# Kernel tuning notes

Measured on AMD Instinct MI355X. Metric: run time of the kernel, lower is better.

The kernel has to match this reference:

```python
import jax, jax.numpy as jnp
import numpy as np

WINDOW = 128  # window_size from init_kwargs
D = 1024      # input_dim
S = 8192      # seq_len


def setup_inputs() -> dict:
    key = jax.random.key(0)
    k1, k2, k3, k4, k5 = jax.random.split(key, 5)
    bound = 1.0 / np.sqrt(D)
    x = jax.random.normal(k1, (1, S, D), dtype=jnp.float32)
    Wq = jax.random.uniform(k2, (D, D), minval=-bound, maxval=bound, dtype=jnp.float32)
    bq = jax.random.uniform(k3, (D,), minval=-bound, maxval=bound, dtype=jnp.float32)
    Wk = jax.random.uniform(k4, (D, D), minval=-bound, maxval=bound, dtype=jnp.float32)
    bk = jax.random.uniform(k5, (D,), minval=-bound, maxval=bound, dtype=jnp.float32)
    return {"x": x, "Wq": Wq, "bq": bq, "Wk": Wk, "bk": bk}


def reference(x, Wq, bq, Wk, bk):
    # x: [1, S, D]  (original code only works with batch==1)
    xs = x[0]                          # [S, D]
    q = xs @ Wq.T + bq                 # [S, D]
    k = xs @ Wk.T + bk                 # [S, D]
    scores = q @ k.T                   # [S, S] dense, matches original buffer
    t = jnp.arange(S)[:, None]
    s = jnp.arange(S)[None, :]
    # original writes scores only for s in [t-WINDOW, t+WINDOW); elsewhere stays 0
    inwin = (s >= t - WINDOW) & (s < t + WINDOW)
    scores = jnp.where(inwin, scores, 0.0)
    attn = jax.nn.softmax(scores, axis=1)  # softmax INCLUDES the zero entries, as in original
    out = attn @ xs                    # [S, D]
    return out
```

## Files before the change

kernel.cpp:

```cpp
#include <hip/hip_runtime.h>

#define S 8192
#define D 1024
#define WINDOW 128
#define TQ 16
#define UMAX 288
#define BK 32
#define PAD 68
#define BAND 320

typedef __attribute__((ext_vector_type(8))) short short8;
typedef __attribute__((ext_vector_type(4))) float floatx4;
typedef __attribute__((ext_vector_type(4))) unsigned short ushort4v;
typedef unsigned short u16t;

__device__ __forceinline__ float wave_sum(float v) {
  #pragma unroll
  for (int off = 32; off > 0; off >>= 1) v += __shfl_xor(v, off, 64);
  return v;
}
__device__ __forceinline__ float wave_max(float v) {
  #pragma unroll
  for (int off = 32; off > 0; off >>= 1) v = fmaxf(v, __shfl_xor(v, off, 64));
  return v;
}
__device__ __forceinline__ unsigned int f2bf_rn(float f) {
  unsigned int u = __float_as_uint(f);
  return (u + 0x7fffu + ((u >> 16) & 1u)) >> 16;
}

#define GLDS(gp, lp) __builtin_amdgcn_global_load_lds( \
    (const __attribute__((address_space(1))) void*)(gp), \
    (__attribute__((address_space(3))) void*)(lp), 16, 0, 0)


__global__ __launch_bounds__(256) void wuv_kernel(
    const float* __restrict__ Wq, const float* __restrict__ Wk,
    const float* __restrict__ bq, const float* __restrict__ bk,
    float* __restrict__ u, float* __restrict__ v, float* __restrict__ cbuf,
    u16t* __restrict__ wqth, u16t* __restrict__ wqtl,
    u16t* __restrict__ wkth, u16t* __restrict__ wktl)
{
  __shared__ float tile[64][65];
  const int t = threadIdx.x;
  if (blockIdx.z == 2) {
    if (blockIdx.x >= 4 || blockIdx.y >= 8) return;
    const int i = blockIdx.x * 256 + t;
    const int n0 = blockIdx.y * 128;
    float us = 0.f, vs = 0.f;
    for (int n = n0; n < n0 + 128; ++n) {
      us += Wq[(size_t)n * D + i] * bk[n];
      vs += Wk[(size_t)n * D + i] * bq[n];
    }
    atomicAdd(&u[i], us);
    atomicAdd(&v[i], vs);
    if (blockIdx.x == 0 && blockIdx.y == 0) {
      float cs = 0.f;
      for (int n = t; n < D; n += 256) cs += bq[n] * bk[n];
      atomicAdd(cbuf, cs);
    }
    return;
  }
  const float* W = blockIdx.z ? Wk : Wq;
  u16t* oh = blockIdx.z ? wkth : wqth;
  u16t* ol = blockIdx.z ? wktl : wqtl;
  const int n0 = blockIdx.x * 64;
  const int i0 = blockIdx.y * 64;
  #pragma unroll
  for (int p = 0; p < 4; ++p) {
    int r = (t >> 4) + p * 16;
    int c = (t & 15) * 4;
    float4 vv = *(const float4*)(W + (size_t)(n0 + r) * D + i0 + c);
    tile[r][c+0] = vv.x; tile[r][c+1] = vv.y; tile[r][c+2] = vv.z; tile[r][c+3] = vv.w;
  }
  __syncthreads();
  #pragma unroll
  for (int p = 0; p < 4; ++p) {
    int ii = (t >> 4) + p * 16;
    int nn = (t & 15) * 4;
    ushort4v h, l;
    #pragma unroll
    for (int e = 0; e < 4; ++e) {
      float f = tile[nn + e][ii];
      unsigned int hb = f2bf_rn(f);
      float hf = __uint_as_float(hb << 16);
      h[e] = (u16t)hb;
      l[e] = (u16t)f2bf_rn(f - hf);
    }
    size_t idx = (size_t)(i0 + ii) * D + n0 + nn;
    *(ushort4v*)(oh + idx) = h;
    *(ushort4v*)(ol + idx) = l;
  }
}

__global__ __launch_bounds__(256) void prep_kernel(
    const float* __restrict__ x, const float* __restrict__ u,
    const float* __restrict__ v, u16t* __restrict__ xhi, u16t* __restrict__ xlo,
    u16t* __restrict__ xT, float* __restrict__ xsum,
    float* __restrict__ a, float* __restrict__ b)
{
  __shared__ float tile[64][65];
  const int s0 = blockIdx.x * 64;
  const int d0 = blockIdx.y * 64;
  const int t = threadIdx.x;
  #pragma unroll
  for (int p = 0; p < 4; ++p) {
    int r = (t >> 4) + p * 16;
    int c = (t & 15) * 4;
    float4 vv = *(const float4*)(x + (size_t)(s0 + r) * D + d0 + c);
    float f[4] = {vv.x, vv.y, vv.z, vv.w};
    tile[r][c+0] = vv.x; tile[r][c+1] = vv.y; tile[r][c+2] = vv.z; tile[r][c+3] = vv.w;
    ushort4v h, l;
    #pragma unroll
    for (int e = 0; e < 4; ++e) {
      unsigned int hb = f2bf_rn(f[e]);
      float hf = __uint_as_float(hb << 16);
      h[e] = (u16t)hb;
      l[e] = (u16t)f2bf_rn(f[e] - hf);
    }
    size_t idx = (size_t)(s0 + r) * D + d0 + c;
    *(ushort4v*)(xhi + idx) = h;
    *(ushort4v*)(xlo + idx) = l;
  }
  __syncthreads();
  #pragma unroll
  for (int p = 0; p < 4; ++p) {
    int dd = (t >> 4) + p * 16;
    int ss = (t & 15) * 4;
    ushort4v o;
    #pragma unroll
    for (int e = 0; e < 4; ++e) o[e] = (u16t)f2bf_rn(tile[ss + e][dd]);
    *(ushort4v*)(xT + (size_t)(d0 + dd) * S + s0 + ss) = o;
  }
  if (t < 64) {
    float s = 0.f;
    #pragma unroll 8
    for (int r = 0; r < 64; ++r) s += tile[r][t];
    atomicAdd(&xsum[d0 + t], s);
  } else if (t < 128) {
    int r = t - 64;
    float s = 0.f;
    for (int c = 0; c < 64; ++c) s += tile[r][c] * u[d0 + c];
    atomicAdd(&a[s0 + r], s);
  } else if (t < 192) {
    int r = t - 128;
    float s = 0.f;
    for (int c = 0; c < 64; ++c) s += tile[r][c] * v[d0 + c];
    atomicAdd(&b[s0 + r], s);
  }
}

__global__ __launch_bounds__(256) void m_kernel(
    const u16t* __restrict__ wqth, const u16t* __restrict__ wqtl,
    const u16t* __restrict__ wkth, const u16t* __restrict__ wktl,
    u16t* __restrict__ mh, u16t* __restrict__ ml)
{
  __shared__ __align__(16) u16t Mbuf[4][64 * BK];

  const int tid  = threadIdx.x;
  const int lane = tid & 63;
  const int wv   = tid >> 6;
  const int i0   = blockIdx.x * 64;
  const int j0   = blockIdx.y * 64;

  floatx4 acc[2][2] = {};
  const int m0w = (wv & 1) * 32;
  const int n0w = (wv >> 1) * 32;
  const int srow = lane >> 2;
  const int scolw = ((lane & 3) ^ ((lane >> 3) & 3)) * 8;
  const int rs    = (((lane >> 4) ^ ((lane >> 1) & 3)) * 8);

  for (int k0 = 0; k0 < D; k0 += BK) {
    __syncthreads();
    {
      const u16t* src = (wv == 0) ? wqth : (wv == 1) ? wqtl : (wv == 2) ? wkth : wktl;
      const int base  = (wv < 2) ? i0 : j0;
      #pragma unroll
      for (int sg = 0; sg < 4; ++sg) {
        int row = base + sg * 16 + srow;
        size_t g = (size_t)row * D + k0 + scolw;
        GLDS(src + g, &Mbuf[wv][sg * 512]);
      }
    }
    __syncthreads();
    short8 ah[2], al[2], bh[2], bl[2];
    #pragma unroll
    for (int t = 0; t < 2; ++t) {
      int ar = (m0w + t * 16 + (lane & 15)) * BK + rs;
      int br = (n0w + t * 16 + (lane & 15)) * BK + rs;
      ah[t] = *(const short8*)&Mbuf[0][ar];
      al[t] = *(const short8*)&Mbuf[1][ar];
      bh[t] = *(const short8*)&Mbuf[2][br];
      bl[t] = *(const short8*)&Mbuf[3][br];
    }
    #pragma unroll
    for (int mt = 0; mt < 2; ++mt)
      #pragma unroll
      for (int nt = 0; nt < 2; ++nt) {
        acc[mt][nt] = __builtin_amdgcn_mfma_f32_16x16x32_bf16(ah[mt], bh[nt], acc[mt][nt], 0, 0, 0);
        acc[mt][nt] = __builtin_amdgcn_mfma_f32_16x16x32_bf16(ah[mt], bl[nt], acc[mt][nt], 0, 0, 0);
        acc[mt][nt] = __builtin_amdgcn_mfma_f32_16x16x32_bf16(al[mt], bh[nt], acc[mt][nt], 0, 0, 0);
      }
  }
  #pragma unroll
  for (int mt = 0; mt < 2; ++mt)
    #pragma unroll
    for (int nt = 0; nt < 2; ++nt) {
      int j = j0 + n0w + nt * 16 + (lane & 15);
      int i = i0 + m0w + mt * 16 + (lane >> 4) * 4;
      #pragma unroll
      for (int r = 0; r < 4; ++r) {
        float f = acc[mt][nt][r];
        unsigned int hb = f2bf_rn(f);
        float hf = __uint_as_float(hb << 16);
        size_t idx = (size_t)(i + r) * D + j;
        mh[idx] = (u16t)hb;
        ml[idx] = (u16t)f2bf_rn(f - hf);
      }
    }
}

__global__ __launch_bounds__(256) void y_kernel(
    const u16t* __restrict__ xhi, const u16t* __restrict__ xlo,
    const u16t* __restrict__ mhp, const u16t* __restrict__ mlp,
    u16t* __restrict__ yh, u16t* __restrict__ yl)
{
  __shared__ __align__(16) u16t Ah[2 * 128 * BK];
  __shared__ __align__(16) u16t Al[2 * 128 * BK];
  __shared__ __align__(16) u16t Bh[2 * 128 * BK];
  __shared__ __align__(16) u16t Bl[2 * 128 * BK];

  const int tid  = threadIdx.x;
  const int lane = tid & 63;
  const int wv   = tid >> 6;
  const int s0   = blockIdx.x * 128;
  const int i0   = blockIdx.y * 128;

  floatx4 acc[4][4] = {};
  const int m0w  = (wv & 1) * 64;
  const int n0w  = (wv >> 1) * 64;
  const int srow = lane >> 2;
  const int scolw = ((lane & 3) ^ ((lane >> 3) & 3)) * 8;
  const int rs    = (((lane >> 4) ^ ((lane >> 1) & 3)) * 8);

  for (int k0 = 0; k0 < D; k0 += 64) {
    __syncthreads();
    #pragma unroll
    for (int h = 0; h < 2; ++h) {
      #pragma unroll
      for (int sg = 0; sg < 2; ++sg) {
        int seg  = wv * 2 + sg;
        int arow = s0 + seg * 16 + srow;
        int brow = i0 + seg * 16 + srow;
        size_t ga = (size_t)arow * D + k0 + h * 32 + scolw;
        size_t gb = (size_t)brow * D + k0 + h * 32 + scolw;
        int lb = h * 4096 + seg * 512;
        GLDS(xhi + ga, &Ah[lb]);
        GLDS(xlo + ga, &Al[lb]);
        GLDS(mhp + gb, &Bh[lb]);
        GLDS(mlp + gb, &Bl[lb]);
      }
    }
    __syncthreads();
    #pragma unroll
    for (int h = 0; h < 2; ++h) {
      short8 ah[4], al[4], bh[4], bl[4];
      #pragma unroll
      for (int t = 0; t < 4; ++t) {
        int ar = h * 4096 + (m0w + t * 16 + (lane & 15)) * BK + rs;
        int br = h * 4096 + (n0w + t * 16 + (lane & 15)) * BK + rs;
        ah[t] = *(const short8*)&Ah[ar];
        al[t] = *(const short8*)&Al[ar];
        bh[t] = *(const short8*)&Bh[br];
        bl[t] = *(const short8*)&Bl[br];
      }
      #pragma unroll
      for (int mt = 0; mt < 4; ++mt)
        #pragma unroll
        for (int nt = 0; nt < 4; ++nt) {
          acc[mt][nt] = __builtin_amdgcn_mfma_f32_16x16x32_bf16(ah[mt], bh[nt], acc[mt][nt], 0, 0, 0);
          acc[mt][nt] = __builtin_amdgcn_mfma_f32_16x16x32_bf16(ah[mt], bl[nt], acc[mt][nt], 0, 0, 0);
          acc[mt][nt] = __builtin_amdgcn_mfma_f32_16x16x32_bf16(al[mt], bh[nt], acc[mt][nt], 0, 0, 0);
        }
    }
  }
  #pragma unroll
  for (int mt = 0; mt < 4; ++mt)
    #pragma unroll
    for (int nt = 0; nt < 4; ++nt) {
      int i = i0 + n0w + nt * 16 + (lane & 15);
      int s = s0 + m0w + mt * 16 + (lane >> 4) * 4;
      #pragma unroll
      for (int r = 0; r < 4; ++r) {
        float f = acc[mt][nt][r];
        unsigned int hb = f2bf_rn(f);
        float hf = __uint_as_float(hb << 16);
        size_t idx = (size_t)(s + r) * D + i;
        yh[idx] = (u16t)hb;
        yl[idx] = (u16t)f2bf_rn(f - hf);
      }
    }
}

__global__ __launch_bounds__(256) void scores_kernel(
    const u16t* __restrict__ xhi, const u16t* __restrict__ xlo,
    const u16t* __restrict__ yh, const u16t* __restrict__ yl,
    const float* __restrict__ a, const float* __restrict__ b,
    const float* __restrict__ cbuf, float* __restrict__ band)
{
  __shared__ __align__(16) u16t Ah[2 * 64 * BK];
  __shared__ __align__(16) u16t Al[2 * 64 * BK];
  __shared__ __align__(16) u16t Bh[2 * 64 * BK];
  __shared__ __align__(16) u16t Bl[2 * 64 * BK];

  const int tid  = threadIdx.x;
  const int lane = tid & 63;
  const int wv   = tid >> 6;
  const int t0   = blockIdx.x * 64;
  const int jt   = blockIdx.y;
  const int s_base = t0 - 128 + jt * 64;
  const float cval = cbuf[0];

  floatx4 acc[2][2] = {};
  const int m0w  = (wv & 1) * 32;
  const int n0w  = (wv >> 1) * 32;
  const int srow = lane >> 2;
  const int scolw = ((lane & 3) ^ ((lane >> 3) & 3)) * 8;
  const int rs    = (((lane >> 4) ^ ((lane >> 1) & 3)) * 8);

  for (int k0 = 0; k0 < D; k0 += 64) {
    __syncthreads();
    #pragma unroll
    for (int h = 0; h < 2; ++h) {
      int arow = t0 + wv * 16 + srow;
      int brow = s_base + wv * 16 + srow;
      brow = min(max(brow, 0), S - 1);
      size_t ga = (size_t)arow * D + k0 + h * 32 + scolw;
      size_t gb = (size_t)brow * D + k0 + h * 32 + scolw;
      int lb = h * 2048 + wv * 512;
      GLDS(xhi + ga, &Ah[lb]);
      GLDS(xlo + ga, &Al[lb]);
      GLDS(yh + gb, &Bh[lb]);
      GLDS(yl + gb, &Bl[lb]);
    }
    __syncthreads();
    #pragma unroll
    for (int h = 0; h < 2; ++h) {
      short8 ah[2], al[2], bh[2], bl[2];
      #pragma unroll
      for (int t = 0; t < 2; ++t) {
        int ar = h * 2048 + (m0w + t * 16 + (lane & 15)) * BK + rs;
        int br = h * 2048 + (n0w + t * 16 + (lane & 15)) * BK + rs;
        ah[t] = *(const short8*)&Ah[ar];
        al[t] = *(const short8*)&Al[ar];
        bh[t] = *(const short8*)&Bh[br];
        bl[t] = *(const short8*)&Bl[br];
      }
      #pragma unroll
      for (int mt = 0; mt < 2; ++mt)
        #pragma unroll
        for (int nt = 0; nt < 2; ++nt) {
          acc[mt][nt] = __builtin_amdgcn_mfma_f32_16x16x32_bf16(ah[mt], bh[nt], acc[mt][nt], 0, 0, 0);
          acc[mt][nt] = __builtin_amdgcn_mfma_f32_16x16x32_bf16(ah[mt], bl[nt], acc[mt][nt], 0, 0, 0);
          acc[mt][nt] = __builtin_amdgcn_mfma_f32_16x16x32_bf16(al[mt], bh[nt], acc[mt][nt], 0, 0, 0);
        }
    }
  }
  #pragma unroll
  for (int mt = 0; mt < 2; ++mt)
    #pragma unroll
    for (int nt = 0; nt < 2; ++nt) {
      int n_loc = n0w + nt * 16 + (lane & 15);
      int s = s_base + n_loc;
      float bv = (s >= 0 && s < S) ? b[s] : 0.f;
      #pragma unroll
      for (int r = 0; r < 4; ++r) {
        int m_loc = m0w + mt * 16 + (lane >> 4) * 4 + r;
        int t = t0 + m_loc;
        bool inwin = (s >= t - WINDOW) && (s < t + WINDOW) && (s >= 0) && (s < S);
        float sv = inwin ? (acc[mt][nt][r] + a[t] + bv + cval) : 0.f;
        band[(size_t)t * BAND + jt * 64 + n_loc] = sv;
      }
    }
}

__global__ __launch_bounds__(256) void softmax_kernel(
    const float* __restrict__ band, u16t* __restrict__ Pb, float* __restrict__ e0d)
{
  const int lane = threadIdx.x & 63;
  const int w    = threadIdx.x >> 6;
  const int t    = blockIdx.x * 4 + w;
  const float* row = band + (size_t)t * BAND;
  float v[5];
  float mx = 0.f;
  #pragma unroll
  for (int i = 0; i < 5; ++i) {
    v[i] = row[i * 64 + lane];
    mx = fmaxf(mx, v[i]);
  }
  mx = wave_max(mx);
  float e0 = __expf(-mx);
  float ss = 0.f;
  #pragma unroll
  for (int i = 0; i < 5; ++i) {
    v[i] = __expf(v[i] - mx);
    ss += v[i];
  }
  ss = wave_sum(ss);
  float dinv = 1.f / (ss + (float)(S - BAND) * e0);
  #pragma unroll
  for (int i = 0; i < 5; ++i)
    Pb[(size_t)t * BAND + i * 64 + lane] = (u16t)f2bf_rn((v[i] - e0) * dinv);
  if (lane == 0) e0d[t] = e0 * dinv;
}

__global__ __launch_bounds__(256) void pv_kernel(
    const u16t* __restrict__ Pb, const u16t* __restrict__ xT,
    const float* __restrict__ e0d, const float* __restrict__ xsum,
    float* __restrict__ out)
{
  __shared__ __align__(16) u16t Ab[2 * 64 * BK];
  __shared__ __align__(16) u16t Bb[2 * 128 * BK];

  const int tid  = threadIdx.x;
  const int lane = tid & 63;
  const int wv   = tid >> 6;
  const int t0   = blockIdx.x * 64;
  const int d0   = blockIdx.y * 128;
  const int origin = t0 - 128;

  floatx4 acc[2][4] = {};
  const int m0w  = (wv & 1) * 32;
  const int n0w  = (wv >> 1) * 64;
  const int srow = lane >> 2;
  const int scolw = ((lane & 3) ^ ((lane >> 3) & 3)) * 8;
  const int rs    = (((lane >> 4) ^ ((lane >> 1) & 3)) * 8);

  for (int k0 = 0; k0 < BAND; k0 += 64) {
    __syncthreads();
    #pragma unroll
    for (int h = 0; h < 2; ++h) {
      {
        int arow = t0 + wv * 16 + srow;
        size_t ga = (size_t)arow * BAND + k0 + h * 32 + scolw;
        int lb = h * 2048 + wv * 512;
        GLDS(Pb + ga, &Ab[lb]);
      }
      #pragma unroll
      for (int sg = 0; sg < 2; ++sg) {
        int seg  = wv * 2 + sg;
        int brow = d0 + seg * 16 + srow;
        int s_g  = origin + k0 + h * 32 + scolw;
        s_g = min(max(s_g, 0), S - 8);
        size_t gb = (size_t)brow * S + s_g;
        int lb = h * 4096 + seg * 512;
        GLDS(xT + gb, &Bb[lb]);
      }
    }
    __syncthreads();
    #pragma unroll
    for (int h = 0; h < 2; ++h) {
      short8 af[2], bf[4];
      #pragma unroll
      for (int t = 0; t < 2; ++t) {
        int ar = h * 2048 + (m0w + t * 16 + (lane & 15)) * BK + rs;
        af[t] = *(const short8*)&Ab[ar];
      }
      #pragma unroll
      for (int t = 0; t < 4; ++t) {
        int br = h * 4096 + (n0w + t * 16 + (lane & 15)) * BK + rs;
        bf[t] = *(const short8*)&Bb[br];
      }
      #pragma unroll
      for (int mt = 0; mt < 2; ++mt)
        #pragma unroll
        for (int nt = 0; nt < 4; ++nt)
          acc[mt][nt] = __builtin_amdgcn_mfma_f32_16x16x32_bf16(af[mt], bf[nt], acc[mt][nt], 0, 0, 0);
    }
  }
  #pragma unroll
  for (int mt = 0; mt < 2; ++mt)
    #pragma unroll
    for (int nt = 0; nt < 4; ++nt) {
      int n_g = d0 + n0w + nt * 16 + (lane & 15);
      float xs = xsum[n_g];
      #pragma unroll
      for (int r = 0; r < 4; ++r) {
        int m_g = t0 + m0w + mt * 16 + (lane >> 4) * 4 + r;
        out[(size_t)m_g * D + n_g] = acc[mt][nt][r] + e0d[m_g] * xs;
      }
    }
}

__global__ __launch_bounds__(256) void proj_kernel(
    const float* __restrict__ x, const float* __restrict__ Wq,
    const float* __restrict__ bqv, const float* __restrict__ Wk,
    const float* __restrict__ bkv, float* __restrict__ qout,
    float* __restrict__ kout)
{
  __shared__ __align__(16) float xs[BK][PAD];
  __shared__ __align__(16) float wqs[BK][PAD];
  __shared__ __align__(16) float wks[BK][PAD];
  const int tid = threadIdx.x;
  const int tx = tid & 15, ty = tid >> 4;
  const int t0 = blockIdx.x * 64, i0 = blockIdx.y * 64;
  float accq[4][4] = {}, acck[4][4] = {};
  const int lrow0 = tid >> 3, lc4 = (tid & 7) * 4;
  for (int k0 = 0; k0 < D; k0 += BK) {
    __syncthreads();
    #pragma unroll
    for (int p = 0; p < 2; ++p) {
      int row = lrow0 + p * 32;
      float4 a = *(const float4*)(x  + (size_t)(t0 + row) * D + k0 + lc4);
      float4 b = *(const float4*)(Wq + (size_t)(i0 + row) * D + k0 + lc4);
      float4 c = *(const float4*)(Wk + (size_t)(i0 + row) * D + k0 + lc4);
      xs [lc4+0][row]=a.x; xs [lc4+1][row]=a.y; xs [lc4+2][row]=a.z; xs [lc4+3][row]=a.w;
      wqs[lc4+0][row]=b.x; wqs[lc4+1][row]=b.y; wqs[lc4+2][row]=b.z; wqs[lc4+3][row]=b.w;
      wks[lc4+0][row]=c.x; wks[lc4+1][row]=c.y; wks[lc4+2][row]=c.z; wks[lc4+3][row]=c.w;
    }
    __syncthreads();
    #pragma unroll
    for (int kk = 0; kk < BK; ++kk) {
      float4 av = *(const float4*)&xs [kk][ty*4];
      float4 bv = *(const float4*)&wqs[kk][tx*4];
      float4 cv = *(const float4*)&wks[kk][tx*4];
      float a[4] = {av.x, av.y, av.z, av.w};
      float b[4] = {bv.x, bv.y, bv.z, bv.w};
      float c[4] = {cv.x, cv.y, cv.z, cv.w};
      #pragma unroll
      for (int r = 0; r < 4; ++r)
        #pragma unroll
        for (int cc = 0; cc < 4; ++cc) {
          accq[r][cc] = fmaf(a[r], b[cc], accq[r][cc]);
          acck[r][cc] = fmaf(a[r], c[cc], acck[r][cc]);
        }
    }
  }
  float4 bq4 = *(const float4*)(bqv + i0 + tx*4);
  float4 bk4 = *(const float4*)(bkv + i0 + tx*4);
  #pragma unroll
  for (int r = 0; r < 4; ++r) {
    int trow = t0 + ty*4 + r;
    float4 oq = { accq[r][0]+bq4.x, accq[r][1]+bq4.y, accq[r][2]+bq4.z, accq[r][3]+bq4.w };
    float4 ok = { acck[r][0]+bk4.x, acck[r][1]+bk4.y, acck[r][2]+bk4.z, acck[r][3]+bk4.w };
    *(float4*)(qout + (size_t)trow * D + i0 + tx*4) = oq;
// ... 109 lines not shown
          acc[ti].z = fmaf(wvv[u], xr[u].z, acc[ti].z);
          acc[ti].w = fmaf(wvv[u], xr[u].w, acc[ti].w);
        }
      }
    }
    float4 xsv = *(const float4*)(xsum + c4);
    #pragma unroll
    for (int ti = 0; ti < TQ; ++ti) {
      float e0 = e0s[ti], di = dinv[ti];
      float4 o;
      o.x = (acc[ti].x + e0 * xsv.x) * di;
      o.y = (acc[ti].y + e0 * xsv.y) * di;
      o.z = (acc[ti].z + e0 * xsv.z) * di;
      o.w = (acc[ti].w + e0 * xsv.w) * di;
      *(float4*)(out + (size_t)(t0 + ti) * D + c4) = o;
    }
  }
}

extern "C" void kernel_launch(void* const* d_in, const int* in_sizes, int n_in,
                              void* d_out, int out_size, void* d_ws, size_t ws_size,
                              hipStream_t stream) {
  const float* x  = (const float*)d_in[0];
  const float* Wq = (const float*)d_in[1];
  const float* bq = (const float*)d_in[2];
  const float* Wk = (const float*)d_in[3];
  const float* bk = (const float*)d_in[4];
  float* outp = (float*)d_out;

  const size_t SD = (size_t)S * D;
  const size_t DD = (size_t)D * D;

  float* xsum = (float*)d_ws;
  float* u    = xsum + D;
  float* v    = u + D;
  float* a    = v + D;
  float* b    = a + S;
  float* cbuf = b + S;
  size_t zero_bytes = (size_t)(3 * D + 2 * S + 16) * sizeof(float);

  u16t* xhi  = (u16t*)(cbuf + 16);
  u16t* xlo  = xhi + SD;
  u16t* xT   = xlo + SD;
  u16t* wqth = xT + SD;
  u16t* wqtl = wqth + DD;
  u16t* wkth = wqtl + DD;
  u16t* wktl = wkth + DD;
  u16t* mh   = wktl + DD;
  u16t* ml   = mh + DD;
  u16t* yh   = ml + DD;
  u16t* yl   = yh + SD;
  float* band = (float*)(yl + SD);
  u16t*  Pb   = (u16t*)(band + (size_t)S * BAND);
  float* e0d  = (float*)(Pb + (size_t)S * BAND);
  size_t needed = (size_t)((char*)(e0d + S) - (char*)d_ws);

  if (ws_size >= needed) {
    (void)hipMemsetAsync(d_ws, 0, zero_bytes, stream);
    wuv_kernel<<<dim3(D / 64, D / 64, 3), 256, 0, stream>>>(
        Wq, Wk, bq, bk, u, v, cbuf, wqth, wqtl, wkth, wktl);
    prep_kernel<<<dim3(S / 64, D / 64), 256, 0, stream>>>(x, u, v, xhi, xlo, xT, xsum, a, b);
    m_kernel<<<dim3(D / 64, D / 64), 256, 0, stream>>>(wqth, wqtl, wkth, wktl, mh, ml);
    y_kernel<<<dim3(S / 128, D / 128), 256, 0, stream>>>(xhi, xlo, mh, ml, yh, yl);
    scores_kernel<<<dim3(S / 64, 5), 256, 0, stream>>>(xhi, xlo, yh, yl, a, b, cbuf, band);
    softmax_kernel<<<S / 4, 256, 0, stream>>>(band, Pb, e0d);
    pv_kernel<<<dim3(S / 64, D / 128), 256, 0, stream>>>(Pb, xT, e0d, xsum, outp);
  } else {
    float* xs2  = (float*)d_ws;
    float* q    = xs2 + D;
    float* kbuf = q + SD;
    (void)hipMemsetAsync(xs2, 0, D * sizeof(float), stream);
    colsum_kernel<<<dim3(D / 256, S / 256), 256, 0, stream>>>(x, xs2);
    proj_kernel<<<dim3(S / 64, D / 64), 256, 0, stream>>>(x, Wq, bq, Wk, bk, q, kbuf);
    attn_kernel<<<S / TQ, 256, 0, stream>>>(x, q, kbuf, xs2, outp);
  }
}
```

Measured before the change: 261.0 us.

## Fuse pipeline stages into one persistent cooperative kernel with grid syncs

Replaces the memset and seven separate kernel launches with a single cooperative persistent kernel of 512 blocks that loops over virtual block indices for each stage, separated by grid-wide syncs. Zeroing moves in-kernel and the m/uv stage is scheduled alongside the transpose stage differently. The aim is to remove launch gaps and tail effects between the short stages. In exchange, the 64KB shared buffer and two-blocks-per-CU bound may reduce occupancy for stages that previously used less LDS, and grid syncs add barrier cost; the separate launches remain as a fallback if the cooperative launch fails.

```diff
diff --git a/kernel.cpp b/kernel.cpp
--- a/kernel.cpp
+++ b/kernel.cpp
@@ -1,4 +1,7 @@
 #include <hip/hip_runtime.h>
+#include <hip/hip_cooperative_groups.h>
+
+namespace cg = cooperative_groups;
 
 #define S 8192
 #define D 1024
@@ -14,6 +17,14 @@
 typedef __attribute__((ext_vector_type(4))) unsigned short ushort4v;
 typedef unsigned short u16t;
 
+struct Params {
+  const float *x, *Wq, *bq, *Wk, *bk;
+  float *out;
+  float *xsum, *u, *v, *a, *b, *cbuf;
+  u16t *xhi, *xlo, *xT, *wqth, *wqtl, *wkth, *wktl, *mh, *ml, *yh, *yl;
+  float *band; u16t *Pb; float *e0d;
+};
+
 __device__ __forceinline__ float wave_sum(float v) {
   #pragma unroll
   for (int off = 32; off > 0; off >>= 1) v += __shfl_xor(v, off, 64);
@@ -34,49 +45,48 @@
     (__attribute__((address_space(3))) void*)(lp), 16, 0, 0)
 
 
-__global__ __launch_bounds__(256) void wuv_kernel(
-    const float* __restrict__ Wq, const float* __restrict__ Wk,
-    const float* __restrict__ bq, const float* __restrict__ bk,
-    float* __restrict__ u, float* __restrict__ v, float* __restrict__ cbuf,
-    u16t* __restrict__ wqth, u16t* __restrict__ wqtl,
-    u16t* __restrict__ wkth, u16t* __restrict__ wktl)
-{
-  __shared__ float tile[64][65];
-  const int t = threadIdx.x;
-  if (blockIdx.z == 2) {
-    if (blockIdx.x >= 4 || blockIdx.y >= 8) return;
-    const int i = blockIdx.x * 256 + t;
-    const int n0 = blockIdx.y * 128;
-    float us = 0.f, vs = 0.f;
-    for (int n = n0; n < n0 + 128; ++n) {
-      us += Wq[(size_t)n * D + i] * bk[n];
-      vs += Wk[(size_t)n * D + i] * bq[n];
-    }
-    atomicAdd(&u[i], us);
-    atomicAdd(&v[i], vs);
-    if (blockIdx.x == 0 && blockIdx.y == 0) {
-      float cs = 0.f;
-      for (int n = t; n < D; n += 256) cs += bq[n] * bk[n];
-      atomicAdd(cbuf, cs);
-    }
-    return;
-  }
-  const float* W = blockIdx.z ? Wk : Wq;
-  u16t* oh = blockIdx.z ? wkth : wqth;
-  u16t* ol = blockIdx.z ? wktl : wqtl;
-  const int n0 = blockIdx.x * 64;
-  const int i0 = blockIdx.y * 64;
-  #pragma unroll
-  for (int p = 0; p < 4; ++p) {
-    int r = (t >> 4) + p * 16;
+
+static __device__ __forceinline__ void zero_body(const Params& p, int zb, int tid) {
+  const int total = 3 * D + 2 * S + 16;
+  for (int i = zb * 256 + tid; i < total; i += 32 * 256) p.xsum[i] = 0.f;
+}
+
+static __device__ __forceinline__ void uv_body(const Params& p, int bx, int by, int tid) {
+  const int i = bx * 256 + tid;
+  const int n0 = by * 128;
+  float us = 0.f, vs = 0.f;
+  for (int n = n0; n < n0 + 128; ++n) {
+    us += p.Wq[(size_t)n * D + i] * p.bk[n];
+    vs += p.Wk[(size_t)n * D + i] * p.bq[n];
+  }
+  atomicAdd(&p.u[i], us);
+  atomicAdd(&p.v[i], vs);
+  if (bx == 0 && by == 0) {
+    float cs = 0.f;
+    for (int n = tid; n < D; n += 256) cs += p.bq[n] * p.bk[n];
+    atomicAdd(p.cbuf, cs);
+  }
+}
+
+static __device__ __forceinline__ void transW_body(
+    const float* __restrict__ W, u16t* __restrict__ oh, u16t* __restrict__ ol,
+    void* sm, int bx, int by, int t)
+{
+  float (*tile)[65] = reinterpret_cast<float (*)[65]>(sm);
+  const int n0 = bx * 64;
+  const int i0 = by * 64;
+  __syncthreads();
+  #pragma unroll
+  for (int pp = 0; pp < 4; ++pp) {
+    int r = (t >> 4) + pp * 16;
     int c = (t & 15) * 4;
     float4 vv = *(const float4*)(W + (size_t)(n0 + r) * D + i0 + c);
     tile[r][c+0] = vv.x; tile[r][c+1] = vv.y; tile[r][c+2] = vv.z; tile[r][c+3] = vv.w;
   }
   __syncthreads();
   #pragma unroll
-  for (int p = 0; p < 4; ++p) {
-    int ii = (t >> 4) + p * 16;
+  for (int pp = 0; pp < 4; ++pp) {
+    int ii = (t >> 4) + pp * 16;
     int nn = (t & 15) * 4;
     ushort4v h, l;
     #pragma unroll
@@ -93,21 +103,18 @@
   }
 }
 
-__global__ __launch_bounds__(256) void prep_kernel(
-    const float* __restrict__ x, const float* __restrict__ u,
-    const float* __restrict__ v, u16t* __restrict__ xhi, u16t* __restrict__ xlo,
-    u16t* __restrict__ xT, float* __restrict__ xsum,
-    float* __restrict__ a, float* __restrict__ b)
-{
-  __shared__ float tile[64][65];
-  const int s0 = blockIdx.x * 64;
-  const int d0 = blockIdx.y * 64;
-  const int t = threadIdx.x;
-  #pragma unroll
-  for (int p = 0; p < 4; ++p) {
-    int r = (t >> 4) + p * 16;
+static __device__ __forceinline__ void prep_body(const Params& p, void* sm,
+                                                 int bx, int by, int t)
+{
+  float (*tile)[65] = reinterpret_cast<float (*)[65]>(sm);
+  const int s0 = bx * 64;
+  const int d0 = by * 64;
+  __syncthreads();
+  #pragma unroll
+  for (int pp = 0; pp < 4; ++pp) {
+    int r = (t >> 4) + pp * 16;
     int c = (t & 15) * 4;
-    float4 vv = *(const float4*)(x + (size_t)(s0 + r) * D + d0 + c);
+    float4 vv = *(const float4*)(p.x + (size_t)(s0 + r) * D + d0 + c);
     float f[4] = {vv.x, vv.y, vv.z, vv.w};
     tile[r][c+0] = vv.x; tile[r][c+1] = vv.y; tile[r][c+2] = vv.z; tile[r][c+3] = vv.w;
     ushort4v h, l;
@@ -119,49 +126,45 @@
       l[e] = (u16t)f2bf_rn(f[e] - hf);
     }
     size_t idx = (size_t)(s0 + r) * D + d0 + c;
-    *(ushort4v*)(xhi + idx) = h;
-    *(ushort4v*)(xlo + idx) = l;
+    *(ushort4v*)(p.xhi + idx) = h;
+    *(ushort4v*)(p.xlo + idx) = l;
   }
   __syncthreads();
   #pragma unroll
-  for (int p = 0; p < 4; ++p) {
-    int dd = (t >> 4) + p * 16;
+  for (int pp = 0; pp < 4; ++pp) {
+    int dd = (t >> 4) + pp * 16;
     int ss = (t & 15) * 4;
     ushort4v o;
     #pragma unroll
     for (int e = 0; e < 4; ++e) o[e] = (u16t)f2bf_rn(tile[ss + e][dd]);
-    *(ushort4v*)(xT + (size_t)(d0 + dd) * S + s0 + ss) = o;
+    *(ushort4v*)(p.xT + (size_t)(d0 + dd) * S + s0 + ss) = o;
   }
   if (t < 64) {
     float s = 0.f;
     #pragma unroll 8
     for (int r = 0; r < 64; ++r) s += tile[r][t];
-    atomicAdd(&xsum[d0 + t], s);
+    atomicAdd(&p.xsum[d0 + t], s);
   } else if (t < 128) {
     int r = t - 64;
     float s = 0.f;
-    for (int c = 0; c < 64; ++c) s += tile[r][c] * u[d0 + c];
-    atomicAdd(&a[s0 + r], s);
+    for (int c = 0; c < 64; ++c) s += tile[r][c] * p.u[d0 + c];
+    atomicAdd(&p.a[s0 + r], s);
   } else if (t < 192) {
     int r = t - 128;
     float s = 0.f;
-    for (int c = 0; c < 64; ++c) s += tile[r][c] * v[d0 + c];
-    atomicAdd(&b[s0 + r], s);
-  }
-}
-
-__global__ __launch_bounds__(256) void m_kernel(
-    const u16t* __restrict__ wqth, const u16t* __restrict__ wqtl,
-    const u16t* __restrict__ wkth, const u16t* __restrict__ wktl,
-    u16t* __restrict__ mh, u16t* __restrict__ ml)
-{
-  __shared__ __align__(16) u16t Mbuf[4][64 * BK];
-
-  const int tid  = threadIdx.x;
+    for (int c = 0; c < 64; ++c) s += tile[r][c] * p.v[d0 + c];
+    atomicAdd(&p.b[s0 + r], s);
+  }
+}
+
+static __device__ __forceinline__ void m_body(const Params& p, void* sm,
+                                              int bx, int by, int tid)
+{
+  u16t (*Mbuf)[64 * BK] = reinterpret_cast<u16t (*)[64 * BK]>(sm);
   const int lane = tid & 63;
   const int wv   = tid >> 6;
-  const int i0   = blockIdx.x * 64;
-  const int j0   = blockIdx.y * 64;
+  const int i0   = bx * 64;
+  const int j0   = by * 64;
 
   floatx4 acc[2][2] = {};
   const int m0w = (wv & 1) * 32;
@@ -173,7 +176,7 @@
   for (int k0 = 0; k0 < D; k0 += BK) {
     __syncthreads();
     {
-      const u16t* src = (wv == 0) ? wqth : (wv == 1) ? wqtl : (wv == 2) ? wkth : wktl;
+      const u16t* src = (wv == 0) ? p.wqth : (wv == 1) ? p.wqtl : (wv == 2) ? p.wkth : p.wktl;
       const int base  = (wv < 2) ? i0 : j0;
       #pragma unroll
       for (int sg = 0; sg < 4; ++sg) {
@@ -214,27 +217,24 @@
         unsigned int hb = f2bf_rn(f);
         float hf = __uint_as_float(hb << 16);
         size_t idx = (size_t)(i + r) * D + j;
-        mh[idx] = (u16t)hb;
-        ml[idx] = (u16t)f2bf_rn(f - hf);
-      }
-    }
-}
-
-__global__ __launch_bounds__(256) void y_kernel(
-    const u16t* __restrict__ xhi, const u16t* __restrict__ xlo,
-    const u16t* __restrict__ mhp, const u16t* __restrict__ mlp,
-    u16t* __restrict__ yh, u16t* __restrict__ yl)
-{
-  __shared__ __align__(16) u16t Ah[2 * 128 * BK];
-  __shared__ __align__(16) u16t Al[2 * 128 * BK];
-  __shared__ __align__(16) u16t Bh[2 * 128 * BK];
-  __shared__ __align__(16) u16t Bl[2 * 128 * BK];
-
-  const int tid  = threadIdx.x;
+        p.mh[idx] = (u16t)hb;
+        p.ml[idx] = (u16t)f2bf_rn(f - hf);
+      }
+    }
+}
+
+static __device__ __forceinline__ void y_body(const Params& p, void* sm,
+                                              int bx, int by, int tid)
+{
+  u16t* Ah = (u16t*)sm;
+  u16t* Al = Ah + 8192;
+  u16t* Bh = Al + 8192;
+  u16t* Bl = Bh + 8192;
+
   const int lane = tid & 63;
   const int wv   = tid >> 6;
-  const int s0   = blockIdx.x * 128;
-  const int i0   = blockIdx.y * 128;
+  const int s0   = bx * 128;
+  const int i0   = by * 128;
 
   floatx4 acc[4][4] = {};
   const int m0w  = (wv & 1) * 64;
@@ -255,10 +255,10 @@
         size_t ga = (size_t)arow * D + k0 + h * 32 + scolw;
         size_t gb = (size_t)brow * D + k0 + h * 32 + scolw;
         int lb = h * 4096 + seg * 512;
-        GLDS(xhi + ga, &Ah[lb]);
-        GLDS(xlo + ga, &Al[lb]);
-        GLDS(mhp + gb, &Bh[lb]);
-        GLDS(mlp + gb, &Bl[lb]);
+        GLDS(p.xhi + ga, &Ah[lb]);
+        GLDS(p.xlo + ga, &Al[lb]);
+        GLDS(p.mh  + gb, &Bh[lb]);
+        GLDS(p.ml  + gb, &Bl[lb]);
       }
     }
     __syncthreads();
@@ -296,30 +296,25 @@
         unsigned int hb = f2bf_rn(f);
         float hf = __uint_as_float(hb << 16);
         size_t idx = (size_t)(s + r) * D + i;
-        yh[idx] = (u16t)hb;
-        yl[idx] = (u16t)f2bf_rn(f - hf);
-      }
-    }
-}
-
-__global__ __launch_bounds__(256) void scores_kernel(
-    const u16t* __restrict__ xhi, const u16t* __restrict__ xlo,
-    const u16t* __restrict__ yh, const u16t* __restrict__ yl,
-    const float* __restrict__ a, const float* __restrict__ b,
-    const float* __restrict__ cbuf, float* __restrict__ band)
-{
-  __shared__ __align__(16) u16t Ah[2 * 64 * BK];
-  __shared__ __align__(16) u16t Al[2 * 64 * BK];
-  __shared__ __align__(16) u16t Bh[2 * 64 * BK];
-  __shared__ __align__(16) u16t Bl[2 * 64 * BK];
-
-  const int tid  = threadIdx.x;
+        p.yh[idx] = (u16t)hb;
+        p.yl[idx] = (u16t)f2bf_rn(f - hf);
+      }
+    }
+}
+
+static __device__ __forceinline__ void scores_body(const Params& p, void* sm,
+                                                   int bx, int jt, int tid)
+{
+  u16t* Ah = (u16t*)sm;
+  u16t* Al = Ah + 4096;
+  u16t* Bh = Al + 4096;
+  u16t* Bl = Bh + 4096;
+
   const int lane = tid & 63;
   const int wv   = tid >> 6;
-  const int t0   = blockIdx.x * 64;
-  const int jt   = blockIdx.y;
+  const int t0   = bx * 64;
   const int s_base = t0 - 128 + jt * 64;
-  const float cval = cbuf[0];
+  const float cval = p.cbuf[0];
 
   floatx4 acc[2][2] = {};
   const int m0w  = (wv & 1) * 32;
@@ -338,10 +333,10 @@
       size_t ga = (size_t)arow * D + k0 + h * 32 + scolw;
       size_t gb = (size_t)brow * D + k0 + h * 32 + scolw;
       int lb = h * 2048 + wv * 512;
-      GLDS(xhi + ga, &Ah[lb]);
-      GLDS(xlo + ga, &Al[lb]);
-      GLDS(yh + gb, &Bh[lb]);
-      GLDS(yl + gb, &Bl[lb]);
+      GLDS(p.xhi + ga, &Ah[lb]);
+      GLDS(p.xlo + ga, &Al[lb]);
+      GLDS(p.yh  + gb, &Bh[lb]);
+      GLDS(p.yl  + gb, &Bl[lb]);
     }
     __syncthreads();
     #pragma unroll
@@ -372,25 +367,24 @@
     for (int nt = 0; nt < 2; ++nt) {
       int n_loc = n0w + nt * 16 + (lane & 15);
       int s = s_base + n_loc;
-      float bv = (s >= 0 && s < S) ? b[s] : 0.f;
+      float bv = (s >= 0 && s < S) ? p.b[s] : 0.f;
       #pragma unroll
       for (int r = 0; r < 4; ++r) {
         int m_loc = m0w + mt * 16 + (lane >> 4) * 4 + r;
         int t = t0 + m_loc;
         bool inwin = (s >= t - WINDOW) && (s < t + WINDOW) && (s >= 0) && (s < S);
-        float sv = inwin ? (acc[mt][nt][r] + a[t] + bv + cval) : 0.f;
-        band[(size_t)t * BAND + jt * 64 + n_loc] = sv;
-      }
-    }
-}
-
-__global__ __launch_bounds__(256) void softmax_kernel(
-    const float* __restrict__ band, u16t* __restrict__ Pb, float* __restrict__ e0d)
-{
-  const int lane = threadIdx.x & 63;
-  const int w    = threadIdx.x >> 6;
-  const int t    = blockIdx.x * 4 + w;
-  const float* row = band + (size_t)t * BAND;
+        float sv = inwin ? (acc[mt][nt][r] + p.a[t] + bv + cval) : 0.f;
+        p.band[(size_t)t * BAND + jt * 64 + n_loc] = sv;
+      }
+    }
+}
+
+static __device__ __forceinline__ void softmax_body(const Params& p, int vb, int tid)
+{
+  const int lane = tid & 63;
+  const int w    = tid >> 6;
+  const int t    = vb * 4 + w;
+  const float* row = p.band + (size_t)t * BAND;
   float v[5];
   float mx = 0.f;
   #pragma unroll
@@ -410,23 +404,20 @@
   float dinv = 1.f / (ss + (float)(S - BAND) * e0);
   #pragma unroll
   for (int i = 0; i < 5; ++i)
-    Pb[(size_t)t * BAND + i * 64 + lane] = (u16t)f2bf_rn((v[i] - e0) * dinv);
-  if (lane == 0) e0d[t] = e0 * dinv;
-}
-
-__global__ __launch_bounds__(256) void pv_kernel(
-    const u16t* __restrict__ Pb, const u16t* __restrict__ xT,
-    const float* __restrict__ e0d, const float* __restrict__ xsum,
-    float* __restrict__ out)
-{
-  __shared__ __align__(16) u16t Ab[2 * 64 * BK];
-  __shared__ __align__(16) u16t Bb[2 * 128 * BK];
-
-  const int tid  = threadIdx.x;
+    p.Pb[(size_t)t * BAND + i * 64 + lane] = (u16t)f2bf_rn((v[i] - e0) * dinv);
+  if (lane == 0) p.e0d[t] = e0 * dinv;
+}
+
+static __device__ __forceinline__ void pv_body(const Params& p, void* sm,
+                                               int bx, int by, int tid)
+{
+  u16t* Ab = (u16t*)sm;
+  u16t* Bb = Ab + 4096;
+
   const int lane = tid & 63;
   const int wv   = tid >> 6;
-  const int t0   = blockIdx.x * 64;
-  const int d0   = blockIdx.y * 128;
+  const int t0   = bx * 64;
+  const int d0   = by * 128;
   const int origin = t0 - 128;
 
   floatx4 acc[2][4] = {};
@@ -444,7 +435,7 @@
         int arow = t0 + wv * 16 + srow;
         size_t ga = (size_t)arow * BAND + k0 + h * 32 + scolw;
         int lb = h * 2048 + wv * 512;
-        GLDS(Pb + ga, &Ab[lb]);
+        GLDS(p.Pb + ga, &Ab[lb]);
       }
       #pragma unroll
       for (int sg = 0; sg < 2; ++sg) {
@@ -454,7 +445,7 @@
         s_g = min(max(s_g, 0), S - 8);
         size_t gb = (size_t)brow * S + s_g;
         int lb = h * 4096 + seg * 512;
-        GLDS(xT + gb, &Bb[lb]);
+        GLDS(p.xT + gb, &Bb[lb]);
       }
     }
     __syncthreads();
@@ -483,13 +474,75 @@
     #pragma unroll
     for (int nt = 0; nt < 4; ++nt) {
       int n_g = d0 + n0w + nt * 16 + (lane & 15);
-      float xs = xsum[n_g];
+      float xs = p.xsum[n_g];
       #pragma unroll
       for (int r = 0; r < 4; ++r) {
         int m_g = t0 + m0w + mt * 16 + (lane >> 4) * 4 + r;
-        out[(size_t)m_g * D + n_g] = acc[mt][nt][r] + e0d[m_g] * xs;
-      }
-    }
+        p.out[(size_t)m_g * D + n_g] = acc[mt][nt][r] + p.e0d[m_g] * xs;
+      }
+    }
+}
+
+__global__ __launch_bounds__(256, 2) void mega_kernel(Params p)
+{
+  __shared__ __align__(16) unsigned char sm[65536];
+  cg::grid_group grid = cg::this_grid();
+  const int tid = threadIdx.x;
+  const int NB  = gridDim.x;
+
+  for (int vb = blockIdx.x; vb < 544; vb += NB) {
+    if (vb < 256)      transW_body(p.Wq, p.wqth, p.wqtl, sm, vb & 15, vb >> 4, tid);
+    else if (vb < 512) transW_body(p.Wk, p.wkth, p.wktl, sm, (vb - 256) & 15, (vb - 256) >> 4, tid);
+    else               zero_body(p, vb - 512, tid);
+  }
+  grid.sync();
+  for (int vb = blockIdx.x; vb < 288; vb += NB) {
+    if (vb < 256) m_body(p, sm, vb & 15, vb >> 4, tid);
+    else          uv_body(p, (vb - 256) & 3, (vb - 256) >> 2, tid);
+  }
+  grid.sync();
+  for (int vb = blockIdx.x; vb < 2048; vb += NB) prep_body(p, sm, vb & 127, vb >> 7, tid);
+  grid.sync();
+  for (int vb = blockIdx.x; vb < 512; vb += NB) y_body(p, sm, vb & 63, vb >> 6, tid);
+  grid.sync();
+  for (int vb = blockIdx.x; vb < 640; vb += NB) scores_body(p, sm, vb & 127, vb >> 7, tid);
+  grid.sync();
+  for (int vb = blockIdx.x; vb < 2048; vb += NB) softmax_body(p, vb, tid);
+  grid.sync();
+  for (int vb = blockIdx.x; vb < 1024; vb += NB) pv_body(p, sm, vb & 127, vb >> 7, tid);
+}
+
+__global__ __launch_bounds__(256) void wuv_g(Params p) {
+  __shared__ __align__(16) unsigned char sm[64 * 65 * 4 + 16];
+  if (blockIdx.z == 2) {
+    if (blockIdx.x < 4 && blockIdx.y < 8) uv_body(p, blockIdx.x, blockIdx.y, threadIdx.x);
+    return;
+  }
+  if (blockIdx.z == 1) transW_body(p.Wk, p.wkth, p.wktl, sm, blockIdx.x, blockIdx.y, threadIdx.x);
+  else                 transW_body(p.Wq, p.wqth, p.wqtl, sm, blockIdx.x, blockIdx.y, threadIdx.x);
+}
+__global__ __launch_bounds__(256) void prep_g(Params p) {
+  __shared__ __align__(16) unsigned char sm[64 * 65 * 4 + 16];
+  prep_body(p, sm, blockIdx.x, blockIdx.y, threadIdx.x);
+}
+__global__ __launch_bounds__(256) void m_g(Params p) {
+  __shared__ __align__(16) unsigned char sm[4 * 64 * BK * 2];
+  m_body(p, sm, blockIdx.x, blockIdx.y, threadIdx.x);
+}
+__global__ __launch_bounds__(256) void y_g(Params p) {
+  __shared__ __align__(16) unsigned char sm[65536];
+  y_body(p, sm, blockIdx.x, blockIdx.y, threadIdx.x);
+}
+__global__ __launch_bounds__(256) void scores_g(Params p) {
+  __shared__ __align__(16) unsigned char sm[32768];
+  scores_body(p, sm, blockIdx.x, blockIdx.y, threadIdx.x);
+}
+__global__ __launch_bounds__(256) void softmax_g(Params p) {
+  softmax_body(p, blockIdx.x, threadIdx.x);
+}
+__global__ __launch_bounds__(256) void pv_g(Params p) {
+  __shared__ __align__(16) unsigned char sm[24576];
+  pv_body(p, sm, blockIdx.x, blockIdx.y, threadIdx.x);
 }
 
 __global__ __launch_bounds__(256) void proj_kernel(
@@ -509,8 +562,8 @@
   for (int k0 = 0; k0 < D; k0 += BK) {
     __syncthreads();
     #pragma unroll
-    for (int p = 0; p < 2; ++p) {
-      int row = lrow0 + p * 32;
+    for (int pp = 0; pp < 2; ++pp) {
+      int row = lrow0 + pp * 32;
       float4 a = *(const float4*)(x  + (size_t)(t0 + row) * D + k0 + lc4);
       float4 b = *(const float4*)(Wq + (size_t)(i0 + row) * D + k0 + lc4);
       float4 c = *(const float4*)(Wk + (size_t)(i0 + row) * D + k0 + lc4);
@@ -710,15 +763,28 @@
   size_t needed = (size_t)((char*)(e0d + S) - (char*)d_ws);
 
   if (ws_size >= needed) {
-    (void)hipMemsetAsync(d_ws, 0, zero_bytes, stream);
-    wuv_kernel<<<dim3(D / 64, D / 64, 3), 256, 0, stream>>>(
-        Wq, Wk, bq, bk, u, v, cbuf, wqth, wqtl, wkth, wktl);
-    prep_kernel<<<dim3(S / 64, D / 64), 256, 0, stream>>>(x, u, v, xhi, xlo, xT, xsum, a, b);
-    m_kernel<<<dim3(D / 64, D / 64), 256, 0, stream>>>(wqth, wqtl, wkth, wktl, mh, ml);
-    y_kernel<<<dim3(S / 128, D / 128), 256, 0, stream>>>(xhi, xlo, mh, ml, yh, yl);
-    scores_kernel<<<dim3(S / 64, 5), 256, 0, stream>>>(xhi, xlo, yh, yl, a, b, cbuf, band);
-    softmax_kernel<<<S / 4, 256, 0, stream>>>(band, Pb, e0d);
-    pv_kernel<<<dim3(S / 64, D / 128), 256, 0, stream>>>(Pb, xT, e0d, xsum, outp);
+    Params P;
+    P.x = x; P.Wq = Wq; P.bq = bq; P.Wk = Wk; P.bk = bk; P.out = outp;
+    P.xsum = xsum; P.u = u; P.v = v; P.a = a; P.b = b; P.cbuf = cbuf;
+    P.xhi = xhi; P.xlo = xlo; P.xT = xT;
+    P.wqth = wqth; P.wqtl = wqtl; P.wkth = wkth; P.wktl = wktl;
+    P.mh = mh; P.ml = ml; P.yh = yh; P.yl = yl;
+    P.band = band; P.Pb = Pb; P.e0d = e0d;
+
+    void* kargs[] = { (void*)&P };
+    hipError_t ce = hipLaunchCooperativeKernel(
+        (const void*)mega_kernel, dim3(512), dim3(256), kargs, 0, stream);
+    if (ce != hipSuccess) {
+      (void)hipGetLastError();
+      (void)hipMemsetAsync(d_ws, 0, zero_bytes, stream);
+      wuv_g<<<dim3(16, 16, 3), 256, 0, stream>>>(P);
+      prep_g<<<dim3(128, 16), 256, 0, stream>>>(P);
+      m_g<<<dim3(16, 16), 256, 0, stream>>>(P);
+      y_g<<<dim3(64, 8), 256, 0, stream>>>(P);
+      scores_g<<<dim3(128, 5), 256, 0, stream>>>(P);
+      softmax_g<<<2048, 256, 0, stream>>>(P);
+      pv_g<<<dim3(128, 8), 256, 0, stream>>>(P);
+    }
   } else {
     float* xs2  = (float*)d_ws;
     float* q    = xs2 + D;
```

Result: slower. 641.0 us (+145.6%).

## Fuse softmax into PV kernel and fold memset into wuv kernel

Applied to the files above, without the earlier changes.

Drops the separate softmax kernel. Each PV block now computes softmax for its 64 rows straight from the fp32 band and writes the bf16 probabilities into LDS, so the Pb and e0d round trip through global memory and one launch go away. The memset is also removed. wuv_kernel zeroes xsum, a and b, writes u and v as two non-atomic partial sums that prep_kernel adds together, and writes the bias constant directly. The cost is that softmax is recomputed in each of the 8 d-column blocks, and the pv_kernel needs about 42KB of LDS, which may lower its occupancy.

```diff
diff --git a/kernel.cpp b/kernel.cpp
--- a/kernel.cpp
+++ b/kernel.cpp
@@ -37,27 +37,38 @@
 __global__ __launch_bounds__(256) void wuv_kernel(
     const float* __restrict__ Wq, const float* __restrict__ Wk,
     const float* __restrict__ bq, const float* __restrict__ bk,
-    float* __restrict__ u, float* __restrict__ v, float* __restrict__ cbuf,
+    float* __restrict__ uu, float* __restrict__ vv, float* __restrict__ cbuf,
     u16t* __restrict__ wqth, u16t* __restrict__ wqtl,
-    u16t* __restrict__ wkth, u16t* __restrict__ wktl)
+    u16t* __restrict__ wkth, u16t* __restrict__ wktl,
+    float* __restrict__ zreg)
 {
   __shared__ float tile[64][65];
+  __shared__ float cr[4];
   const int t = threadIdx.x;
   if (blockIdx.z == 2) {
-    if (blockIdx.x >= 4 || blockIdx.y >= 8) return;
-    const int i = blockIdx.x * 256 + t;
-    const int n0 = blockIdx.y * 128;
-    float us = 0.f, vs = 0.f;
-    for (int n = n0; n < n0 + 128; ++n) {
-      us += Wq[(size_t)n * D + i] * bk[n];
-      vs += Wk[(size_t)n * D + i] * bq[n];
-    }
-    atomicAdd(&u[i], us);
-    atomicAdd(&v[i], vs);
-    if (blockIdx.x == 0 && blockIdx.y == 0) {
-      float cs = 0.f;
-      for (int n = t; n < D; n += 256) cs += bq[n] * bk[n];
-      atomicAdd(cbuf, cs);
+    if (blockIdx.y == 0) {
+      if (blockIdx.x < 8) {
+        const int i  = (blockIdx.x & 3) * 256 + t;
+        const int nh = blockIdx.x >> 2;
+        float us = 0.f, vs = 0.f;
+        for (int n = nh * 512; n < nh * 512 + 512; ++n) {
+          us += Wq[(size_t)n * D + i] * bk[n];
+          vs += Wk[(size_t)n * D + i] * bq[n];
+        }
+        uu[(size_t)nh * D + i] = us;
+        vv[(size_t)nh * D + i] = vs;
+      } else if (blockIdx.x == 8) {
+        float cs = 0.f;
+        for (int n = t; n < D; n += 256) cs += bq[n] * bk[n];
+        cs = wave_sum(cs);
+        if ((t & 63) == 0) cr[t >> 6] = cs;
+        __syncthreads();
+        if (t == 0) cbuf[0] = cr[0] + cr[1] + cr[2] + cr[3];
+      }
+    } else {
+      int fb  = (blockIdx.y - 1) * 16 + blockIdx.x;
+      int idx = fb * 256 + t;
+      if (idx < D + 2 * S) zreg[idx] = 0.f;
     }
     return;
   }
@@ -70,8 +81,8 @@
   for (int p = 0; p < 4; ++p) {
     int r = (t >> 4) + p * 16;
     int c = (t & 15) * 4;
-    float4 vv = *(const float4*)(W + (size_t)(n0 + r) * D + i0 + c);
-    tile[r][c+0] = vv.x; tile[r][c+1] = vv.y; tile[r][c+2] = vv.z; tile[r][c+3] = vv.w;
+    float4 vf = *(const float4*)(W + (size_t)(n0 + r) * D + i0 + c);
+    tile[r][c+0] = vf.x; tile[r][c+1] = vf.y; tile[r][c+2] = vf.z; tile[r][c+3] = vf.w;
   }
   __syncthreads();
   #pragma unroll
@@ -94,8 +105,8 @@
 }
 
 __global__ __launch_bounds__(256) void prep_kernel(
-    const float* __restrict__ x, const float* __restrict__ u,
-    const float* __restrict__ v, u16t* __restrict__ xhi, u16t* __restrict__ xlo,
+    const float* __restrict__ x, const float* __restrict__ uu,
+    const float* __restrict__ vv, u16t* __restrict__ xhi, u16t* __restrict__ xlo,
     u16t* __restrict__ xT, float* __restrict__ xsum,
     float* __restrict__ a, float* __restrict__ b)
 {
@@ -107,9 +118,9 @@
   for (int p = 0; p < 4; ++p) {
     int r = (t >> 4) + p * 16;
     int c = (t & 15) * 4;
-    float4 vv = *(const float4*)(x + (size_t)(s0 + r) * D + d0 + c);
-    float f[4] = {vv.x, vv.y, vv.z, vv.w};
-    tile[r][c+0] = vv.x; tile[r][c+1] = vv.y; tile[r][c+2] = vv.z; tile[r][c+3] = vv.w;
+    float4 vf = *(const float4*)(x + (size_t)(s0 + r) * D + d0 + c);
+    float f[4] = {vf.x, vf.y, vf.z, vf.w};
+    tile[r][c+0] = vf.x; tile[r][c+1] = vf.y; tile[r][c+2] = vf.z; tile[r][c+3] = vf.w;
     ushort4v h, l;
     #pragma unroll
     for (int e = 0; e < 4; ++e) {
@@ -140,12 +151,12 @@
   } else if (t < 128) {
     int r = t - 64;
     float s = 0.f;
-    for (int c = 0; c < 64; ++c) s += tile[r][c] * u[d0 + c];
+    for (int c = 0; c < 64; ++c) s += tile[r][c] * (uu[d0 + c] + uu[D + d0 + c]);
     atomicAdd(&a[s0 + r], s);
   } else if (t < 192) {
     int r = t - 128;
     float s = 0.f;
-    for (int c = 0; c < 64; ++c) s += tile[r][c] * v[d0 + c];
+    for (int c = 0; c < 64; ++c) s += tile[r][c] * (vv[d0 + c] + vv[D + d0 + c]);
     atomicAdd(&b[s0 + r], s);
   }
 }
@@ -384,43 +395,14 @@
     }
 }
 
-__global__ __launch_bounds__(256) void softmax_kernel(
-    const float* __restrict__ band, u16t* __restrict__ Pb, float* __restrict__ e0d)
-{
-  const int lane = threadIdx.x & 63;
-  const int w    = threadIdx.x >> 6;
-  const int t    = blockIdx.x * 4 + w;
-  const float* row = band + (size_t)t * BAND;
-  float v[5];
-  float mx = 0.f;
-  #pragma unroll
-  for (int i = 0; i < 5; ++i) {
-    v[i] = row[i * 64 + lane];
-    mx = fmaxf(mx, v[i]);
-  }
-  mx = wave_max(mx);
-  float e0 = __expf(-mx);
-  float ss = 0.f;
-  #pragma unroll
-  for (int i = 0; i < 5; ++i) {
-    v[i] = __expf(v[i] - mx);
-    ss += v[i];
-  }
-  ss = wave_sum(ss);
-  float dinv = 1.f / (ss + (float)(S - BAND) * e0);
-  #pragma unroll
-  for (int i = 0; i < 5; ++i)
-    Pb[(size_t)t * BAND + i * 64 + lane] = (u16t)f2bf_rn((v[i] - e0) * dinv);
-  if (lane == 0) e0d[t] = e0 * dinv;
-}
-
+#define PSTR 328
 __global__ __launch_bounds__(256) void pv_kernel(
-    const u16t* __restrict__ Pb, const u16t* __restrict__ xT,
-    const float* __restrict__ e0d, const float* __restrict__ xsum,
-    float* __restrict__ out)
-{
-  __shared__ __align__(16) u16t Ab[2 * 64 * BK];
+    const float* __restrict__ band, const u16t* __restrict__ xT,
+    const float* __restrict__ xsum, float* __restrict__ out)
+{
+  __shared__ __align__(16) u16t Pl[64 * PSTR];
   __shared__ __align__(16) u16t Bb[2 * 128 * BK];
+  __shared__ float e0s[64];
 
   const int tid  = threadIdx.x;
   const int lane = tid & 63;
@@ -429,23 +411,45 @@
   const int d0   = blockIdx.y * 128;
   const int origin = t0 - 128;
 
+  for (int it = 0; it < 16; ++it) {
+    int rloc = it * 4 + wv;
+    const float* row = band + (size_t)(t0 + rloc) * BAND;
+    float v[5];
+    float mx = 0.f;
+    #pragma unroll
+    for (int i = 0; i < 5; ++i) {
+      v[i] = row[i * 64 + lane];
+      mx = fmaxf(mx, v[i]);
+    }
+    mx = wave_max(mx);
+    float e0 = __expf(-mx);
+    float ss = 0.f;
+    #pragma unroll
+    for (int i = 0; i < 5; ++i) {
+      v[i] = __expf(v[i] - mx);
+      ss += v[i];
+    }
+    ss = wave_sum(ss);
+    float dinv = 1.f / (ss + (float)(S - BAND) * e0);
+    #pragma unroll
+    for (int i = 0; i < 5; ++i)
+      Pl[rloc * PSTR + i * 64 + lane] = (u16t)f2bf_rn((v[i] - e0) * dinv);
+    if (lane == 0) e0s[rloc] = e0 * dinv;
+  }
+
   floatx4 acc[2][4] = {};
   const int m0w  = (wv & 1) * 32;
   const int n0w  = (wv >> 1) * 64;
   const int srow = lane >> 2;
   const int scolw = ((lane & 3) ^ ((lane >> 3) & 3)) * 8;
   const int rs    = (((lane >> 4) ^ ((lane >> 1) & 3)) * 8);
+  const int fr    = lane & 15;
+  const int qA    = (lane >> 4) * 8;
 
   for (int k0 = 0; k0 < BAND; k0 += 64) {
     __syncthreads();
     #pragma unroll
     for (int h = 0; h < 2; ++h) {
-      {
-        int arow = t0 + wv * 16 + srow;
-        size_t ga = (size_t)arow * BAND + k0 + h * 32 + scolw;
-        int lb = h * 2048 + wv * 512;
-        GLDS(Pb + ga, &Ab[lb]);
-      }
       #pragma unroll
       for (int sg = 0; sg < 2; ++sg) {
         int seg  = wv * 2 + sg;
@@ -453,8 +457,7 @@
         int s_g  = origin + k0 + h * 32 + scolw;
         s_g = min(max(s_g, 0), S - 8);
         size_t gb = (size_t)brow * S + s_g;
-        int lb = h * 4096 + seg * 512;
-        GLDS(xT + gb, &Bb[lb]);
+        GLDS(xT + gb, &Bb[h * 4096 + seg * 512]);
       }
     }
     __syncthreads();
@@ -462,15 +465,11 @@
     for (int h = 0; h < 2; ++h) {
       short8 af[2], bf[4];
       #pragma unroll
-      for (int t = 0; t < 2; ++t) {
-        int ar = h * 2048 + (m0w + t * 16 + (lane & 15)) * BK + rs;
-        af[t] = *(const short8*)&Ab[ar];
-      }
-      #pragma unroll
-      for (int t = 0; t < 4; ++t) {
-        int br = h * 4096 + (n0w + t * 16 + (lane & 15)) * BK + rs;
-        bf[t] = *(const short8*)&Bb[br];
-      }
+      for (int t = 0; t < 2; ++t)
+        af[t] = *(const short8*)&Pl[(m0w + t * 16 + fr) * PSTR + k0 + h * 32 + qA];
+      #pragma unroll
+      for (int t = 0; t < 4; ++t)
+        bf[t] = *(const short8*)&Bb[h * 4096 + (n0w + t * 16 + fr) * BK + rs];
       #pragma unroll
       for (int mt = 0; mt < 2; ++mt)
         #pragma unroll
@@ -482,12 +481,12 @@
   for (int mt = 0; mt < 2; ++mt)
     #pragma unroll
     for (int nt = 0; nt < 4; ++nt) {
-      int n_g = d0 + n0w + nt * 16 + (lane & 15);
+      int n_g = d0 + n0w + nt * 16 + fr;
       float xs = xsum[n_g];
       #pragma unroll
       for (int r = 0; r < 4; ++r) {
-        int m_g = t0 + m0w + mt * 16 + (lane >> 4) * 4 + r;
-        out[(size_t)m_g * D + n_g] = acc[mt][nt][r] + e0d[m_g] * xs;
+        int rloc = m0w + mt * 16 + (lane >> 4) * 4 + r;
+        out[(size_t)(t0 + rloc) * D + n_g] = acc[mt][nt][r] + e0s[rloc] * xs;
       }
     }
 }
@@ -686,12 +685,11 @@
   const size_t DD = (size_t)D * D;
 
   float* xsum = (float*)d_ws;
-  float* u    = xsum + D;
-  float* v    = u + D;
-  float* a    = v + D;
+  float* a    = xsum + D;
   float* b    = a + S;
-  float* cbuf = b + S;
-  size_t zero_bytes = (size_t)(3 * D + 2 * S + 16) * sizeof(float);
+  float* uu   = b + S;
+  float* vv   = uu + 2 * D;
+  float* cbuf = vv + 2 * D;
 
   u16t* xhi  = (u16t*)(cbuf + 16);
   u16t* xlo  = xhi + SD;
@@ -705,20 +703,16 @@
   u16t* yh   = ml + DD;
   u16t* yl   = yh + SD;
   float* band = (float*)(yl + SD);
-  u16t*  Pb   = (u16t*)(band + (size_t)S * BAND);
-  float* e0d  = (float*)(Pb + (size_t)S * BAND);
-  size_t needed = (size_t)((char*)(e0d + S) - (char*)d_ws);
+  size_t needed = (size_t)((char*)(band + (size_t)S * BAND) - (char*)d_ws);
 
   if (ws_size >= needed) {
-    (void)hipMemsetAsync(d_ws, 0, zero_bytes, stream);
-    wuv_kernel<<<dim3(D / 64, D / 64, 3), 256, 0, stream>>>(
-        Wq, Wk, bq, bk, u, v, cbuf, wqth, wqtl, wkth, wktl);
-    prep_kernel<<<dim3(S / 64, D / 64), 256, 0, stream>>>(x, u, v, xhi, xlo, xT, xsum, a, b);
+    wuv_kernel<<<dim3(16, 16, 3), 256, 0, stream>>>(
+        Wq, Wk, bq, bk, uu, vv, cbuf, wqth, wqtl, wkth, wktl, xsum);
+    prep_kernel<<<dim3(S / 64, D / 64), 256, 0, stream>>>(x, uu, vv, xhi, xlo, xT, xsum, a, b);
     m_kernel<<<dim3(D / 64, D / 64), 256, 0, stream>>>(wqth, wqtl, wkth, wktl, mh, ml);
     y_kernel<<<dim3(S / 128, D / 128), 256, 0, stream>>>(xhi, xlo, mh, ml, yh, yl);
     scores_kernel<<<dim3(S / 64, 5), 256, 0, stream>>>(xhi, xlo, yh, yl, a, b, cbuf, band);
-    softmax_kernel<<<S / 4, 256, 0, stream>>>(band, Pb, e0d);
-    pv_kernel<<<dim3(S / 64, D / 128), 256, 0, stream>>>(Pb, xT, e0d, xsum, outp);
+    pv_kernel<<<dim3(S / 64, D / 128), 256, 0, stream>>>(band, xT, xsum, outp);
   } else {
     float* xs2  = (float*)d_ws;
     float* q    = xs2 + D;
```

New measurement: 293.2 us. 1.12x slower.
